# Kernel optimization log

Measured on AMD Instinct MI355X. Metric: run time of the kernel, lower is better.

Reference implementation:

```python
import jax, jax.numpy as jnp
import numpy as np

EPS = 1e-5
NC = 183  # num_classes
FUSION_LEVEL = 1

def conv2d(x, w, b=None, pad=0):
    y = jax.lax.conv_general_dilated(x, w, (1, 1), [(pad, pad), (pad, pad)],
                                     dimension_numbers=('NCHW', 'OIHW', 'NCHW'))
    return y if b is None else y + b[None, :, None, None]

def bn(x, g, b, m, v):
    s = g / jnp.sqrt(v + EPS)
    return x * s[None, :, None, None] + (b - m * s)[None, :, None, None]

def deform_conv(x, offset, weight):
    # DCNv1: x [B,C,H,W], offset [B,18,H,W] as (dy,dx) per kernel point, weight [O,C,3,3]
    B, C, H, W = x.shape
    K = 9
    off = offset.reshape(B, K, 2, H, W)
    ky = (jnp.arange(K) // 3 - 1).astype(x.dtype)
    kx = (jnp.arange(K) % 3 - 1).astype(x.dtype)
    yy = jnp.arange(H, dtype=x.dtype)[None, None, :, None] + ky[None, :, None, None] + off[:, :, 0]
    xx = jnp.arange(W, dtype=x.dtype)[None, None, None, :] + kx[None, :, None, None] + off[:, :, 1]
    y0 = jnp.floor(yy)
    x0 = jnp.floor(xx)
    wy = yy - y0
    wx = xx - x0
    def gather(yi, xi):
        valid = ((yi >= 0) & (yi <= H - 1) & (xi >= 0) & (xi <= W - 1))
        yc = jnp.clip(yi, 0, H - 1).astype(jnp.int32)
        xc = jnp.clip(xi, 0, W - 1).astype(jnp.int32)
        g = jax.vmap(lambda im, a, b: im[:, a, b])(x, yc, xc)  # [B,C,K,H,W]
        return g * valid.astype(x.dtype)[:, None]
    s = (gather(y0, x0) * ((1 - wy) * (1 - wx))[:, None]
         + gather(y0, x0 + 1) * ((1 - wy) * wx)[:, None]
         + gather(y0 + 1, x0) * (wy * (1 - wx))[:, None]
         + gather(y0 + 1, x0 + 1) * (wy * wx)[:, None])
    return jnp.einsum('bckhw,ock->bohw', s, weight.reshape(weight.shape[0], C, K))

def resize_bilinear(x, oh, ow):
    # F.interpolate(mode='bilinear', align_corners=True)
    B, C, H, W = x.shape
    if (H, W) == (oh, ow):
        return x
    ys = jnp.linspace(0.0, H - 1.0, oh)
    xs = jnp.linspace(0.0, W - 1.0, ow)
    y0 = jnp.clip(jnp.floor(ys).astype(jnp.int32), 0, H - 2)
    x0 = jnp.clip(jnp.floor(xs).astype(jnp.int32), 0, W - 2)
    wy = (ys - y0).astype(x.dtype)
    wx = (xs - x0).astype(x.dtype)
    r = x[:, :, y0, :] * (1 - wy)[None, None, :, None] + x[:, :, y0 + 1, :] * wy[None, None, :, None]
    return r[:, :, :, x0] * (1 - wx) + r[:, :, :, x0 + 1] * wx

def setup_inputs() -> dict:
    key = jax.random.key(0)
    ks = iter(jax.random.split(key, 64))
    nk = lambda: next(ks)
    B, C = 1, 256
    sizes = [256, 128, 64, 32, 16]
    w = lambda shape, sc: jax.random.normal(nk(), shape, jnp.float32) * sc
    inp = {}
    for i, s in enumerate(sizes):
        inp['feat%d' % i] = jax.random.normal(nk(), (B, C, s, s), jnp.float32)
    inp['off1_w'] = w((18, C, 3, 3), 0.01); inp['off1_b'] = w((18,), 0.01)
    inp['dc1_w'] = w((C, C, 3, 3), 0.02)
    inp['off2_w'] = w((18, C, 3, 3), 0.01); inp['off2_b'] = w((18,), 0.01)
    inp['dc2_w'] = w((C, C, 3, 3), 0.02)
    inp['bn2_g'] = 1.0 + w((C,), 0.01); inp['bn2_b'] = w((C,), 0.01)
    inp['bn2_m'] = w((C,), 0.01); inp['bn2_v'] = jax.random.uniform(nk(), (C,), jnp.float32) + 0.5
    inp['convs_w'] = w((4, C, C, 3, 3), 0.02)
    inp['convs_g'] = 1.0 + w((4, C), 0.01); inp['convs_b'] = w((4, C), 0.01)
    inp['convs_m'] = w((4, C), 0.01); inp['convs_v'] = jax.random.uniform(nk(), (4, C), jnp.float32) + 0.5
    inp['emb_w'] = w((C, C, 1, 1), 0.05)
    inp['emb_g'] = 1.0 + w((C,), 0.01); inp['emb_b'] = w((C,), 0.01)
    inp['emb_m'] = w((C,), 0.01); inp['emb_v'] = jax.random.uniform(nk(), (C,), jnp.float32) + 0.5
    inp['logit_w'] = w((NC, C, 1, 1), 0.05); inp['logit_b'] = w((NC,), 0.01)
    return inp

def reference(feat0, feat1, feat2, feat3, feat4,
              off1_w, off1_b, dc1_w, off2_w, off2_b, dc2_w,
              bn2_g, bn2_b, bn2_m, bn2_v,
              convs_w, convs_g, convs_b, convs_m, convs_v,
              emb_w, emb_g, emb_b, emb_m, emb_v,
              logit_w, logit_b):
    feats = [feat0, feat1, feat2, feat3, feat4]
    def branch(f):
        o = conv2d(f, off1_w, off1_b, pad=1)
        h = deform_conv(f, o, dc1_w)
        o = conv2d(h, off2_w, off2_b, pad=1)
        h = deform_conv(h, o, dc2_w)
        return jax.nn.relu(bn(h, bn2_g, bn2_b, bn2_m, bn2_v))
    x = branch(feats[FUSION_LEVEL])
    H, W = x.shape[-2:]
    for i, f in enumerate(feats):
        if i != FUSION_LEVEL:
            x = x + branch(resize_bilinear(f, H, W))
    for i in range(4):
        x = jax.nn.relu(bn(conv2d(x, convs_w[i], pad=1),
                           convs_g[i], convs_b[i], convs_m[i], convs_v[i]))
    mask_pred = conv2d(x, logit_w, logit_b, pad=0)
    emb = jax.nn.relu(bn(conv2d(x, emb_w, pad=0), emb_g, emb_b, emb_m, emb_v))
    return (mask_pred, emb)
```

## Files before the change

### kernel.cpp

```cpp
#include <hip/hip_runtime.h>
#include <hip/hip_bf16.h>
#include <stdint.h>

#define EPS_BN 1e-5f
constexpr int PP = 16384;
using short8 = __attribute__((ext_vector_type(8))) short;
using f32x4  = __attribute__((ext_vector_type(4))) float;
typedef unsigned short u16;

__device__ inline float bf2f(u16 u) {
  unsigned v = ((unsigned)u) << 16; float f; __builtin_memcpy(&f, &v, 4); return f;
}
__device__ inline u16 f2bf(float f) {
  unsigned b; __builtin_memcpy(&b, &f, 4);
  b += 0x7FFFu + ((b >> 16) & 1u);
  return (u16)(b >> 16);
}

#define GLD16(g, l) __builtin_amdgcn_global_load_lds( \
    (__attribute__((address_space(1))) void*)(void*)(g), \
    (__attribute__((address_space(3))) void*)(void*)(l), 16, 0, 0)

__global__ void bn_prep_k(const float* __restrict__ g0, const float* __restrict__ b0,
                          const float* __restrict__ m0, const float* __restrict__ v0,
                          const float* __restrict__ cg, const float* __restrict__ cb,
                          const float* __restrict__ cm, const float* __restrict__ cv,
                          const float* __restrict__ eg, const float* __restrict__ eb,
                          const float* __restrict__ em, const float* __restrict__ ev,
                          float* __restrict__ scale, float* __restrict__ shift) {
  int c = threadIdx.x;
  float s = g0[c] * rsqrtf(v0[c] + EPS_BN);
  scale[c] = s; shift[c] = b0[c] - m0[c] * s;
#pragma unroll
  for (int i = 0; i < 4; ++i) {
    float si = cg[i*256+c] * rsqrtf(cv[i*256+c] + EPS_BN);
    scale[(1+i)*256+c] = si; shift[(1+i)*256+c] = cb[i*256+c] - cm[i*256+c]*si;
  }
  float se = eg[c] * rsqrtf(ev[c] + EPS_BN);
  scale[5*256+c] = se; shift[5*256+c] = eb[c] - em[c]*se;
}

__global__ void prep_w_k(const float* __restrict__ w, u16* __restrict__ W2,
                         int Ocnt, int KK, int NPAD) {
  int idx = blockIdx.x * 256 + threadIdx.x;
  int total = NPAD * KK * 256;
  if (idx >= total) return;
  int o = idx / (KK * 256); int rem = idx - o * (KK * 256);
  int kpt = rem >> 8, c = rem & 255;
  W2[idx] = (o < Ocnt) ? f2bf(w[(o * 256 + c) * KK + kpt]) : (u16)0;
}

__global__ void tr_k(const float* __restrict__ in, u16* __restrict__ out, int P) {
  __shared__ float tile[64][65];
  int p0 = blockIdx.x * 64, c0 = blockIdx.y * 64;
  int t = threadIdx.x;
  int tl = t & 63, tg = t >> 6;
#pragma unroll
  for (int i = 0; i < 16; ++i) {
    int c = tg * 16 + i;
    tile[c][tl] = in[(size_t)(c0 + c) * P + p0 + tl];
  }
  __syncthreads();
  int px = t >> 2, cq = t & 3;
#pragma unroll
  for (int pass = 0; pass < 2; ++pass) {
    int c = cq * 8 + pass * 32;
    u16 r[8];
#pragma unroll
    for (int j = 0; j < 8; ++j) r[j] = f2bf(tile[c + j][px]);
    *(short8*)(out + (size_t)(p0 + px) * 256 + c0 + c) = *(short8*)r;
  }
}

__global__ void rs_k(const u16* __restrict__ in, u16* __restrict__ out, int Hs) {
  int t = threadIdx.x;
  int p = blockIdx.x * 8 + (t >> 5), q = t & 31;
  int oy = p >> 7, ox = p & 127;
  float sc = (float)(Hs - 1) / 127.0f;
  float ys = oy * sc, xs = ox * sc;
  int y0 = (int)ys; if (y0 > Hs - 2) y0 = Hs - 2;
  int x0 = (int)xs; if (x0 > Hs - 2) x0 = Hs - 2;
  float wy = ys - (float)y0, wx = xs - (float)x0;
  const u16* b00 = in + ((size_t)(y0 * Hs + x0)) * 256 + q * 8;
  short8 v00 = *(const short8*)b00;
  short8 v01 = *(const short8*)(b00 + 256);
  short8 v10 = *(const short8*)(b00 + (size_t)Hs * 256);
  short8 v11 = *(const short8*)(b00 + (size_t)Hs * 256 + 256);
  u16 r[8];
#pragma unroll
  for (int j = 0; j < 8; ++j) {
    float a = bf2f((u16)v00[j]) * (1.f - wx) + bf2f((u16)v01[j]) * wx;
    float b = bf2f((u16)v10[j]) * (1.f - wx) + bf2f((u16)v11[j]) * wx;
    r[j] = f2bf(a * (1.f - wy) + b * wy);
  }
  *(short8*)(out + (size_t)p * 256 + q * 8) = *(short8*)r;
}

template<int EPI>
__launch_bounds__(256, 2)
__global__ void dc_k(const u16* __restrict__ A, const u16* __restrict__ Bw,
                     const float* __restrict__ offs, u16* __restrict__ oB,
                     const float* __restrict__ scale, const float* __restrict__ shift) {
  __shared__ u16 sB[2][256 * 32];
  const int t = threadIdx.x, w = t >> 6, l = t & 63, lr = l & 15, lq = l >> 4;
  int bx = blockIdx.x; { int n8 = gridDim.x >> 3; bx = (bx & 7) * n8 + (bx >> 3); }
  const int p0 = bx * 128;
  const int gp0 = p0 + w * 32 + lr, gp1 = gp0 + 16;

  f32x4 acc[2][16];
#pragma unroll
  for (int r = 0; r < 2; ++r)
#pragma unroll
    for (int n = 0; n < 16; ++n) acc[r][n] = (f32x4){0.f, 0.f, 0.f, 0.f};

  float wgt[2][4];
  int   cb[2][4];
  short8 cv[2][4];
  const short8 z8 = (short8){0, 0, 0, 0, 0, 0, 0, 0};

  unsigned boff[4];
#pragma unroll
  for (int it = 0; it < 4; ++it) {
    int ch = it * 256 + t, row = ch >> 2, s = ch & 3;
    int cl = s ^ ((row ^ (row >> 2)) & 3);
    boff[it] = (unsigned)(row * 2304 + cl * 8);
  }

  auto newKpt = [&](int kpt) {
    float2 oa = *(const float2*)(offs + (size_t)gp0 * 32 + 2 * kpt);
    float2 ob = *(const float2*)(offs + (size_t)gp1 * 32 + 2 * kpt);
    float ky = (float)(kpt / 3 - 1), kx = (float)(kpt % 3 - 1);
#pragma unroll
    for (int r = 0; r < 2; ++r) {
      int g = r ? gp1 : gp0;
      float2 o2 = r ? ob : oa;
      int pl = g & 16383, lb = g & ~16383;
      float yy = (float)(pl >> 7) + ky + o2.x;
      float xx = (float)(pl & 127) + kx + o2.y;
      float yf = floorf(yy), xf = floorf(xx);
      float fy = yy - yf, fx = xx - xf;
      int y0 = (int)yf, x0 = (int)xf;
      bool va = (unsigned)y0 < 128u, vb = (unsigned)(y0 + 1) < 128u;
      bool ha = (unsigned)x0 < 128u, hb = (unsigned)(x0 + 1) < 128u;
      wgt[r][0] = (1.f - fy) * (1.f - fx); cb[r][0] = (va && ha) ? lb + (y0 << 7) + x0 : -1;
      wgt[r][1] = (1.f - fy) * fx;         cb[r][1] = (va && hb) ? lb + (y0 << 7) + x0 + 1 : -1;
      wgt[r][2] = fy * (1.f - fx);         cb[r][2] = (vb && ha) ? lb + ((y0 + 1) << 7) + x0 : -1;
      wgt[r][3] = fy * fx;                 cb[r][3] = (vb && hb) ? lb + ((y0 + 1) << 7) + x0 + 1 : -1;
    }
  };
  auto loadC = [&](int ks) {
    int cc = ((ks & 7) << 5) + lq * 8;
#pragma unroll
    for (int r = 0; r < 2; ++r)
#pragma unroll
      for (int c = 0; c < 4; ++c)
        cv[r][c] = (cb[r][c] >= 0) ? *(const short8*)(A + (size_t)cb[r][c] * 256 + cc) : z8;
  };

  newKpt(0);
  loadC(0);
  const int laneoff = lr * 64 + ((lq ^ ((lr ^ (lr >> 2)) & 3)) << 4);

  for (int ks = 0; ks < 72; ++ks) {
    {
      const u16* bbase = Bw + ks * 32;
      char* dst = (char*)sB[ks & 1] + w * 1024;
#pragma unroll
      for (int it = 0; it < 4; ++it) GLD16(bbase + boff[it], dst + it * 4096);
    }
    short8 af[2];
#pragma unroll
    for (int r = 0; r < 2; ++r) {
      u16 rr[8];
#pragma unroll
      for (int j = 0; j < 8; ++j) {
        float v = wgt[r][0] * bf2f((u16)cv[r][0][j]) + wgt[r][1] * bf2f((u16)cv[r][1][j])
                + wgt[r][2] * bf2f((u16)cv[r][2][j]) + wgt[r][3] * bf2f((u16)cv[r][3][j]);
        __hip_bfloat16 h = __float2bfloat16(v);
        rr[j] = *(u16*)&h;
      }
      af[r] = *(short8*)rr;
    }
    if (ks < 71 && (((ks + 1) & 7) == 0)) newKpt((ks + 1) >> 3);
    __syncthreads();
    if (ks < 71) loadC(ks + 1);
    const char* base = (const char*)sB[ks & 1] + laneoff;
    __builtin_amdgcn_s_setprio(1);
#pragma unroll
    for (int n = 0; n < 16; ++n) {
      short8 bfr = *(const short8*)(base + n * 1024);
      acc[0][n] = __builtin_amdgcn_mfma_f32_16x16x32_bf16(af[0], bfr, acc[0][n], 0, 0, 0);
      acc[1][n] = __builtin_amdgcn_mfma_f32_16x16x32_bf16(af[1], bfr, acc[1][n], 0, 0, 0);
    }
    __builtin_amdgcn_s_setprio(0);
  }

#pragma unroll
  for (int r = 0; r < 2; ++r) {
    int prow = p0 + w * 32 + r * 16 + lq * 4;
#pragma unroll
    for (int n = 0; n < 16; ++n) {
      int oc = n * 16 + lr;
      float sc = 1.f, sh = 0.f;
      if constexpr (EPI == 3) { sc = scale[oc]; sh = shift[oc]; }
#pragma unroll
      for (int q = 0; q < 4; ++q) {
        float v = acc[r][n][q];
        if constexpr (EPI == 3) v = fmaxf(v * sc + sh, 0.f);
        oB[(size_t)(prow + q) * 256 + oc] = f2bf(v);
      }
    }
  }
}

template<int MODE, int AM, int AN, int MW, int NW, int EPI>
__launch_bounds__(MW*NW*64)
__global__ void mm_k(const u16* __restrict__ A, const u16* __restrict__ B,
                     const u16* __restrict__ zbuf,
                     float* __restrict__ oF, u16* __restrict__ oB,
                     const float* __restrict__ bias,
                     const float* __restrict__ scale, const float* __restrict__ shift,
                     int Ktot, int ksteps, int OutN) {
  constexpr int BM = MW * AM * 16, BN = NW * AN * 16, NT = MW * NW * 64;
  constexpr int AITS = BM * 8 / NT, BITS = BN * 8 / NT;
  __shared__ u16 sA[BM * 64];
  __shared__ u16 sB[BN * 64];
  char* sAb = (char*)sA; char* sBb = (char*)sB;
  const int t = threadIdx.x;
  const int w = t >> 6, l = t & 63;
  const int lr = l & 15, lq = l >> 4;
  const int wm = w / NW, wn = w % NW;
  int bx = blockIdx.x;
  { int n8 = gridDim.x >> 3; bx = (bx & 7) * n8 + (bx >> 3); }
  const int p0 = bx * BM, n0 = blockIdx.y * BN;

  f32x4 acc[AM][AN];
#pragma unroll
  for (int m = 0; m < AM; ++m)
#pragma unroll
    for (int n = 0; n < AN; ++n) acc[m][n] = (f32x4){0.f, 0.f, 0.f, 0.f};

  for (int ks = 0; ks < ksteps; ++ks) {
    int k0 = ks * 64;
#pragma unroll
    for (int it = 0; it < BITS; ++it) {
      int ch = it * NT + t;
      int row = ch >> 3, cl = (ch & 7) ^ (row & 7);
      GLD16(B + (size_t)(n0 + row) * Ktot + k0 + cl * 8, sBb + it * (NT * 16) + w * 1024);
    }
    if constexpr (MODE == 0) {
#pragma unroll
      for (int it = 0; it < AITS; ++it) {
        int ch = it * NT + t;
        int row = ch >> 3, cl = (ch & 7) ^ (row & 7);
        GLD16(A + (size_t)(p0 + row) * Ktot + k0 + cl * 8, sAb + it * (NT * 16) + w * 1024);
      }
    } else {
      int kpt = k0 >> 8, c0 = k0 & 255;
      int dy = kpt / 3 - 1, dx = kpt % 3 - 1;
#pragma unroll
      for (int it = 0; it < AITS; ++it) {
        int ch = it * NT + t;
        int row = ch >> 3, cl = (ch & 7) ^ (row & 7);
        int gp = p0 + row; int lvl = gp >> 14, pl = gp & 16383;
        int yy = (pl >> 7) + dy, xx = (pl & 127) + dx;
        const u16* src = ((unsigned)yy < 128u && (unsigned)xx < 128u)
            ? A + ((size_t)(lvl << 14) + (yy << 7) + xx) * 256 + c0 + cl * 8
            : zbuf;
        GLD16(src, sAb + it * (NT * 16) + w * 1024);
      }
    }
    __syncthreads();
    short8 af[AM], bfr[AN];
#pragma unroll
    for (int h = 0; h < 2; ++h) {
#pragma unroll
      for (int m = 0; m < AM; ++m) {
        int ar = wm * AM * 16 + m * 16 + lr;
        af[m] = *(const short8*)(sAb + ar * 128 + (((h * 4 + lq) ^ (ar & 7)) << 4));
      }
#pragma unroll
      for (int n = 0; n < AN; ++n) {
        int br = wn * AN * 16 + n * 16 + lr;
        bfr[n] = *(const short8*)(sBb + br * 128 + (((h * 4 + lq) ^ (br & 7)) << 4));
      }
#pragma unroll
      for (int m = 0; m < AM; ++m)
#pragma unroll
        for (int n = 0; n < AN; ++n)
          acc[m][n] = __builtin_amdgcn_mfma_f32_16x16x32_bf16(af[m], bfr[n], acc[m][n], 0, 0, 0);
    }
    __syncthreads();
  }

#pragma unroll
  for (int m = 0; m < AM; ++m) {
    int prow = p0 + wm * AM * 16 + m * 16 + lq * 4;
#pragma unroll
    for (int n = 0; n < AN; ++n) {
      int oc = n0 + wn * AN * 16 + n * 16 + lr;
      if constexpr (EPI == 1) {
        float bs = (oc < 18) ? bias[oc] : 0.f;
#pragma unroll
        for (int r = 0; r < 4; ++r) oF[(size_t)(prow + r) * 32 + oc] = acc[m][n][r] + bs;
      } else if constexpr (EPI == 2) {
#pragma unroll
        for (int r = 0; r < 4; ++r) oB[(size_t)(prow + r) * 256 + oc] = f2bf(acc[m][n][r]);
      } else if constexpr (EPI == 3) {
        float sc = scale[oc], sh = shift[oc];
#pragma unroll
        for (int r = 0; r < 4; ++r)
          oB[(size_t)(prow + r) * 256 + oc] = f2bf(fmaxf(acc[m][n][r] * sc + sh, 0.f));
      } else if constexpr (EPI == 4) {
        if (oc < OutN) {
          float bs = bias[oc];
          float4 v = {acc[m][n][0] + bs, acc[m][n][1] + bs, acc[m][n][2] + bs, acc[m][n][3] + bs};
          *(float4*)(oF + (size_t)oc * PP + prow) = v;
        }
      } else {
        float sc = scale[oc], sh = shift[oc];
        float4 v = {fmaxf(acc[m][n][0] * sc + sh, 0.f), fmaxf(acc[m][n][1] * sc + sh, 0.f),
                    fmaxf(acc[m][n][2] * sc + sh, 0.f), fmaxf(acc[m][n][3] * sc + sh, 0.f)};
        *(float4*)(oF + (size_t)oc * PP + prow) = v;
      }
    }
  }
}

__global__ void sum5_k(const u16* __restrict__ H2, u16* __restrict__ out) {
  size_t base = ((size_t)blockIdx.x * 256 + threadIdx.x) * 8;
  float a[8] = {0,0,0,0,0,0,0,0};
#pragma unroll
  for (int lvl = 0; lvl < 5; ++lvl) {
    short8 v = *(const short8*)(H2 + (size_t)lvl * PP * 256 + base);
#pragma unroll
    for (int j = 0; j < 8; ++j) a[j] += bf2f((u16)v[j]);
  }
  u16 r[8];
#pragma unroll
  for (int j = 0; j < 8; ++j) r[j] = f2bf(a[j]);
  *(short8*)(out + base) = *(short8*)r;
}

extern "C" void kernel_launch(void* const* d_in, const int* in_sizes, int n_in,
                              void* d_out, int out_size, void* d_ws, size_t ws_size,
                              hipStream_t stream) {
  const float* feats[5];
  for (int i = 0; i < 5; ++i) feats[i] = (const float*)d_in[i];
  int fsz[5] = {256, 128, 64, 32, 16};
  const float* off1_w = (const float*)d_in[5];
  const float* off1_b = (const float*)d_in[6];
  const float* dc1_w  = (const float*)d_in[7];
  const float* off2_w = (const float*)d_in[8];
  const float* off2_b = (const float*)d_in[9];
  const float* dc2_w  = (const float*)d_in[10];
  const float* bn2_g  = (const float*)d_in[11];
  const float* bn2_b  = (const float*)d_in[12];
  const float* bn2_m  = (const float*)d_in[13];
  const float* bn2_v  = (const float*)d_in[14];
  const float* convs_w = (const float*)d_in[15];
  const float* convs_g = (const float*)d_in[16];
  const float* convs_b = (const float*)d_in[17];
  const float* convs_m = (const float*)d_in[18];
  const float* convs_v = (const float*)d_in[19];
  const float* emb_w  = (const float*)d_in[20];
  const float* emb_g  = (const float*)d_in[21];
  const float* emb_b  = (const float*)d_in[22];
  const float* emb_m  = (const float*)d_in[23];
  const float* emb_v  = (const float*)d_in[24];
  const float* logit_w = (const float*)d_in[25];
  const float* logit_b = (const float*)d_in[26];

  char* ws = (char*)d_ws;
  size_t off = 0;
  auto alloc = [&](size_t bytes) { char* p = ws + off; off += (bytes + 255) & ~255ull; return p; };
  float* bnscale = (float*)alloc(6 * 256 * 4);
  float* bnshift = (float*)alloc(6 * 256 * 4);
  u16* zbuf = (u16*)alloc(256);
  u16* W2_off1 = (u16*)alloc((size_t)32 * 2304 * 2);
  u16* W2_off2 = (u16*)alloc((size_t)32 * 2304 * 2);
  u16* W2_dc1  = (u16*)alloc((size_t)256 * 2304 * 2);
  u16* W2_dc2  = (u16*)alloc((size_t)256 * 2304 * 2);
  u16* W2_c    = (u16*)alloc((size_t)4 * 256 * 2304 * 2);
  u16* W2_logit = (u16*)alloc((size_t)256 * 256 * 2);
  u16* W2_emb   = (u16*)alloc((size_t)256 * 256 * 2);
  u16* R_all  = (u16*)alloc((size_t)5 * PP * 256 * 2);
  u16* H_all  = (u16*)alloc((size_t)5 * PP * 256 * 2);
  u16* H2_all = (u16*)alloc((size_t)5 * PP * 256 * 2);
  float* O    = (float*)alloc((size_t)5 * PP * 32 * 4);
  u16* Xb     = (u16*)alloc((size_t)PP * 256 * 2);
  u16* Ftmp = H_all;
  u16* cb0 = R_all;
  u16* cb1 = R_all + (size_t)PP * 256;

  hipMemsetAsync(zbuf, 0, 256, stream);
  bn_prep_k<<<1, 256, 0, stream>>>(bn2_g, bn2_b, bn2_m, bn2_v, convs_g, convs_b, convs_m, convs_v,
                                   emb_g, emb_b, emb_m, emb_v, bnscale, bnshift);
  auto pw = [&](const float* src, u16* dst, int Ocnt, int KK, int NPAD) {
    int total = NPAD * KK * 256;
    prep_w_k<<<(total + 255) / 256, 256, 0, stream>>>(src, dst, Ocnt, KK, NPAD);
  };
  pw(off1_w, W2_off1, 18, 9, 32);
  pw(off2_w, W2_off2, 18, 9, 32);
  pw(dc1_w,  W2_dc1, 256, 9, 256);
  pw(dc2_w,  W2_dc2, 256, 9, 256);
  for (int i = 0; i < 4; ++i) pw(convs_w + (size_t)i * 2304 * 256, W2_c + (size_t)i * 2304 * 256, 256, 9, 256);
  pw(logit_w, W2_logit, 183, 1, 256);
  pw(emb_w,   W2_emb,   256, 1, 256);

  const dim3 blk(256);
  for (int lvl = 0; lvl < 5; ++lvl) {
    int P = fsz[lvl] * fsz[lvl];
    u16* dst = (lvl == 1) ? (R_all + (size_t)PP * 256) : Ftmp;
    tr_k<<<dim3(P / 64, 4), blk, 0, stream>>>(feats[lvl], dst, P);
    if (lvl != 1)
      rs_k<<<dim3(PP / 8), blk, 0, stream>>>(Ftmp, R_all + (size_t)lvl * PP * 256, fsz[lvl]);
  }

  constexpr int MG = 5 * PP;
  mm_k<1, 2, 2, 4, 1, 1><<<dim3(MG / 128, 1), blk, 0, stream>>>(
      R_all, W2_off1, zbuf, O, nullptr, off1_b, nullptr, nullptr, 2304, 36, 32);
  dc_k<2><<<dim3(MG / 128), blk, 0, stream>>>(R_all, W2_dc1, O, H_all, nullptr, nullptr);
  mm_k<1, 2, 2, 4, 1, 1><<<dim3(MG / 128, 1), blk, 0, stream>>>(
      H_all, W2_off2, zbuf, O, nullptr, off2_b, nullptr, nullptr, 2304, 36, 32);
  dc_k<3><<<dim3(MG / 128), blk, 0, stream>>>(H_all, W2_dc2, O, H2_all, bnscale, bnshift);

  sum5_k<<<dim3(2048), blk, 0, stream>>>(H2_all, Xb);

  const u16* cur = Xb;
  u16* cbuf[2] = {cb0, cb1};
  for (int i = 0; i < 4; ++i) {
    mm_k<1, 2, 4, 2, 2, 3><<<dim3(PP / 64, 2), blk, 0, stream>>>(
        cur, W2_c + (size_t)i * 2304 * 256, zbuf, nullptr, cbuf[i & 1],
        nullptr, bnscale + (1 + i) * 256, bnshift + (1 + i) * 256, 2304, 36, 256);
    cur = cbuf[i & 1];
  }

  float* outp = (float*)d_out;
  mm_k<0, 2, 4, 2, 2, 4><<<dim3(PP / 64, 2), blk, 0, stream>>>(
      cur, W2_logit, zbuf, outp, nullptr, logit_b, nullptr, nullptr, 256, 4, 183);
  mm_k<0, 2, 4, 2, 2, 5><<<dim3(PP / 64, 2), blk, 0, stream>>>(
      cur, W2_emb, zbuf, outp + (size_t)183 * PP, nullptr, nullptr,
      bnscale + 5 * 256, bnshift + 5 * 256, 256, 4, 256);
}
```

Baseline: 965.7 us.

## Halve deformable-conv tile rows per wave to raise occupancy and prefetch offsets

Each wave of the deformable conv kernel now handles 16 output pixels instead of 32, so a block covers 64 pixels and the grid doubles. Occupancy rises from 2 to 3 blocks per SM. Register pressure drops, and the next kernel point's offset is prefetched one step ahead. Bilinear blending now unpacks bf16 pairs from 32-bit words. The cost is that every weight tile loaded into LDS is reused by half as many MFMAs, which doubles weight traffic per output and lowers MFMA density per sync.

```diff
diff --git a/kernel.cpp b/kernel.cpp
--- a/kernel.cpp
+++ b/kernel.cpp
@@ -97,25 +97,25 @@
 }
 
 template<int EPI>
-__launch_bounds__(256, 2)
+__launch_bounds__(256, 3)
 __global__ void dc_k(const u16* __restrict__ A, const u16* __restrict__ Bw,
                      const float* __restrict__ offs, u16* __restrict__ oB,
                      const float* __restrict__ scale, const float* __restrict__ shift) {
   __shared__ u16 sB[2][256 * 32];
   const int t = threadIdx.x, w = t >> 6, l = t & 63, lr = l & 15, lq = l >> 4;
   int bx = blockIdx.x; { int n8 = gridDim.x >> 3; bx = (bx & 7) * n8 + (bx >> 3); }
-  const int p0 = bx * 128;
-  const int gp0 = p0 + w * 32 + lr, gp1 = gp0 + 16;
-
-  f32x4 acc[2][16];
-#pragma unroll
-  for (int r = 0; r < 2; ++r)
-#pragma unroll
-    for (int n = 0; n < 16; ++n) acc[r][n] = (f32x4){0.f, 0.f, 0.f, 0.f};
-
-  float wgt[2][4];
-  int   cb[2][4];
-  short8 cv[2][4];
+  const int p0 = bx * 64;
+  const int gp = p0 + w * 16 + lr;
+  const int pl = gp & 16383, lb = gp & ~16383;
+
+  f32x4 acc[16];
+#pragma unroll
+  for (int n = 0; n < 16; ++n) acc[n] = (f32x4){0.f, 0.f, 0.f, 0.f};
+
+  float wgt[4];
+  int   cb[4];
+  short8 cv[4];
+  float2 onext;
   const short8 z8 = (short8){0, 0, 0, 0, 0, 0, 0, 0};
 
   unsigned boff[4];
@@ -126,35 +126,28 @@
     boff[it] = (unsigned)(row * 2304 + cl * 8);
   }
 
+  onext = *(const float2*)(offs + (size_t)gp * 32);
+
   auto newKpt = [&](int kpt) {
-    float2 oa = *(const float2*)(offs + (size_t)gp0 * 32 + 2 * kpt);
-    float2 ob = *(const float2*)(offs + (size_t)gp1 * 32 + 2 * kpt);
-    float ky = (float)(kpt / 3 - 1), kx = (float)(kpt % 3 - 1);
-#pragma unroll
-    for (int r = 0; r < 2; ++r) {
-      int g = r ? gp1 : gp0;
-      float2 o2 = r ? ob : oa;
-      int pl = g & 16383, lb = g & ~16383;
-      float yy = (float)(pl >> 7) + ky + o2.x;
-      float xx = (float)(pl & 127) + kx + o2.y;
-      float yf = floorf(yy), xf = floorf(xx);
-      float fy = yy - yf, fx = xx - xf;
-      int y0 = (int)yf, x0 = (int)xf;
-      bool va = (unsigned)y0 < 128u, vb = (unsigned)(y0 + 1) < 128u;
-      bool ha = (unsigned)x0 < 128u, hb = (unsigned)(x0 + 1) < 128u;
-      wgt[r][0] = (1.f - fy) * (1.f - fx); cb[r][0] = (va && ha) ? lb + (y0 << 7) + x0 : -1;
-      wgt[r][1] = (1.f - fy) * fx;         cb[r][1] = (va && hb) ? lb + (y0 << 7) + x0 + 1 : -1;
-      wgt[r][2] = fy * (1.f - fx);         cb[r][2] = (vb && ha) ? lb + ((y0 + 1) << 7) + x0 : -1;
-      wgt[r][3] = fy * fx;                 cb[r][3] = (vb && hb) ? lb + ((y0 + 1) << 7) + x0 + 1 : -1;
-    }
+    float2 o2 = onext;
+    if (kpt < 8) onext = *(const float2*)(offs + (size_t)gp * 32 + 2 * (kpt + 1));
+    float yy = (float)((pl >> 7) + kpt / 3 - 1) + o2.x;
+    float xx = (float)((pl & 127) + kpt % 3 - 1) + o2.y;
+    float yf = floorf(yy), xf = floorf(xx);
+    float fy = yy - yf, fx = xx - xf;
+    int y0 = (int)yf, x0 = (int)xf;
+    bool va = (unsigned)y0 < 128u, vb = (unsigned)(y0 + 1) < 128u;
+    bool ha = (unsigned)x0 < 128u, hb = (unsigned)(x0 + 1) < 128u;
+    wgt[0] = (1.f - fy) * (1.f - fx); cb[0] = (va && ha) ? lb + (y0 << 7) + x0 : -1;
+    wgt[1] = (1.f - fy) * fx;         cb[1] = (va && hb) ? lb + (y0 << 7) + x0 + 1 : -1;
+    wgt[2] = fy * (1.f - fx);         cb[2] = (vb && ha) ? lb + ((y0 + 1) << 7) + x0 : -1;
+    wgt[3] = fy * fx;                 cb[3] = (vb && hb) ? lb + ((y0 + 1) << 7) + x0 + 1 : -1;
   };
   auto loadC = [&](int ks) {
     int cc = ((ks & 7) << 5) + lq * 8;
 #pragma unroll
-    for (int r = 0; r < 2; ++r)
-#pragma unroll
-      for (int c = 0; c < 4; ++c)
-        cv[r][c] = (cb[r][c] >= 0) ? *(const short8*)(A + (size_t)cb[r][c] * 256 + cc) : z8;
+    for (int c = 0; c < 4; ++c)
+      cv[c] = (cb[c] >= 0) ? *(const short8*)(A + (size_t)cb[c] * 256 + cc) : z8;
   };
 
   newKpt(0);
@@ -168,18 +161,37 @@
 #pragma unroll
       for (int it = 0; it < 4; ++it) GLD16(bbase + boff[it], dst + it * 4096);
     }
-    short8 af[2];
-#pragma unroll
-    for (int r = 0; r < 2; ++r) {
+    short8 af;
+    {
       u16 rr[8];
-#pragma unroll
-      for (int j = 0; j < 8; ++j) {
-        float v = wgt[r][0] * bf2f((u16)cv[r][0][j]) + wgt[r][1] * bf2f((u16)cv[r][1][j])
-                + wgt[r][2] * bf2f((u16)cv[r][2][j]) + wgt[r][3] * bf2f((u16)cv[r][3][j]);
-        __hip_bfloat16 h = __float2bfloat16(v);
-        rr[j] = *(u16*)&h;
-      }
-      af[r] = *(short8*)rr;
+      const unsigned* u0 = (const unsigned*)&cv[0];
+      const unsigned* u1 = (const unsigned*)&cv[1];
+      const unsigned* u2 = (const unsigned*)&cv[2];
+      const unsigned* u3 = (const unsigned*)&cv[3];
+#pragma unroll
+      for (int j2 = 0; j2 < 4; ++j2) {
+        float lo, hi;
+        {
+          unsigned a0 = u0[j2], a1 = u1[j2], a2 = u2[j2], a3 = u3[j2];
+          float l0, h0, l1, h1, l2, h2, l3, h3;
+          unsigned tl_, th_;
+          tl_ = a0 << 16; th_ = a0 & 0xFFFF0000u;
+          __builtin_memcpy(&l0, &tl_, 4); __builtin_memcpy(&h0, &th_, 4);
+          tl_ = a1 << 16; th_ = a1 & 0xFFFF0000u;
+          __builtin_memcpy(&l1, &tl_, 4); __builtin_memcpy(&h1, &th_, 4);
+          tl_ = a2 << 16; th_ = a2 & 0xFFFF0000u;
+          __builtin_memcpy(&l2, &tl_, 4); __builtin_memcpy(&h2, &th_, 4);
+          tl_ = a3 << 16; th_ = a3 & 0xFFFF0000u;
+          __builtin_memcpy(&l3, &tl_, 4); __builtin_memcpy(&h3, &th_, 4);
+          lo = wgt[0] * l0 + wgt[1] * l1 + wgt[2] * l2 + wgt[3] * l3;
+          hi = wgt[0] * h0 + wgt[1] * h1 + wgt[2] * h2 + wgt[3] * h3;
+        }
+        __hip_bfloat16 hl = __float2bfloat16(lo);
+        __hip_bfloat16 hh = __float2bfloat16(hi);
+        rr[2 * j2]     = *(u16*)&hl;
+        rr[2 * j2 + 1] = *(u16*)&hh;
+      }
+      af = *(short8*)rr;
     }
     if (ks < 71 && (((ks + 1) & 7) == 0)) newKpt((ks + 1) >> 3);
     __syncthreads();
@@ -189,15 +201,13 @@
 #pragma unroll
     for (int n = 0; n < 16; ++n) {
       short8 bfr = *(const short8*)(base + n * 1024);
-      acc[0][n] = __builtin_amdgcn_mfma_f32_16x16x32_bf16(af[0], bfr, acc[0][n], 0, 0, 0);
-      acc[1][n] = __builtin_amdgcn_mfma_f32_16x16x32_bf16(af[1], bfr, acc[1][n], 0, 0, 0);
+      acc[n] = __builtin_amdgcn_mfma_f32_16x16x32_bf16(af, bfr, acc[n], 0, 0, 0);
     }
     __builtin_amdgcn_s_setprio(0);
   }
 
-#pragma unroll
-  for (int r = 0; r < 2; ++r) {
-    int prow = p0 + w * 32 + r * 16 + lq * 4;
+  {
+    int prow = p0 + w * 16 + lq * 4;
 #pragma unroll
     for (int n = 0; n < 16; ++n) {
       int oc = n * 16 + lr;
@@ -205,7 +215,7 @@
       if constexpr (EPI == 3) { sc = scale[oc]; sh = shift[oc]; }
 #pragma unroll
       for (int q = 0; q < 4; ++q) {
-        float v = acc[r][n][q];
+        float v = acc[n][q];
         if constexpr (EPI == 3) v = fmaxf(v * sc + sh, 0.f);
         oB[(size_t)(prow + q) * 256 + oc] = f2bf(v);
       }
@@ -420,10 +430,10 @@
   constexpr int MG = 5 * PP;
   mm_k<1, 2, 2, 4, 1, 1><<<dim3(MG / 128, 1), blk, 0, stream>>>(
       R_all, W2_off1, zbuf, O, nullptr, off1_b, nullptr, nullptr, 2304, 36, 32);
-  dc_k<2><<<dim3(MG / 128), blk, 0, stream>>>(R_all, W2_dc1, O, H_all, nullptr, nullptr);
+  dc_k<2><<<dim3(MG / 64), blk, 0, stream>>>(R_all, W2_dc1, O, H_all, nullptr, nullptr);
   mm_k<1, 2, 2, 4, 1, 1><<<dim3(MG / 128, 1), blk, 0, stream>>>(
       H_all, W2_off2, zbuf, O, nullptr, off2_b, nullptr, nullptr, 2304, 36, 32);
-  dc_k<3><<<dim3(MG / 128), blk, 0, stream>>>(H_all, W2_dc2, O, H2_all, bnscale, bnshift);
+  dc_k<3><<<dim3(MG / 64), blk, 0, stream>>>(H_all, W2_dc2, O, H2_all, bnscale, bnshift);
 
   sum5_k<<<dim3(2048), blk, 0, stream>>>(H2_all, Xb);
 
```

Result: faster. 879.3 us (-8.9%).

## Triple-buffer weight staging and prefetch offsets in deformable conv kernel

Applied to the files above, without the earlier changes.

Moves the shared-memory weight tiles for the deformable-conv GEMM from double to triple buffering, issuing the LDS DMA for step ks+1 before computing step ks. It also prefetches the next kernel point's offsets one step ahead. The bf16-to-float unpacking of the bilinear samples now works on 32-bit pairs, and the full __syncthreads is replaced by a raw s_barrier plus a sched_barrier. The aim is to hide global-load latency behind the MFMA work and cut barrier overhead. Shared memory per block grows, and the raw barrier may not wait for the outstanding LDS DMA the way the old sync did, which is a correctness risk.

```diff
diff --git a/kernel.cpp b/kernel.cpp
--- a/kernel.cpp
+++ b/kernel.cpp
@@ -101,11 +101,11 @@
 __global__ void dc_k(const u16* __restrict__ A, const u16* __restrict__ Bw,
                      const float* __restrict__ offs, u16* __restrict__ oB,
                      const float* __restrict__ scale, const float* __restrict__ shift) {
-  __shared__ u16 sB[2][256 * 32];
+  __shared__ u16 sB[3][256 * 32];
   const int t = threadIdx.x, w = t >> 6, l = t & 63, lr = l & 15, lq = l >> 4;
   int bx = blockIdx.x; { int n8 = gridDim.x >> 3; bx = (bx & 7) * n8 + (bx >> 3); }
   const int p0 = bx * 128;
-  const int gp0 = p0 + w * 32 + lr, gp1 = gp0 + 16;
+  const int gp0 = p0 + w * 32 + lr;
 
   f32x4 acc[2][16];
 #pragma unroll
@@ -116,6 +116,7 @@
   float wgt[2][4];
   int   cb[2][4];
   short8 cv[2][4];
+  float2 onext[2];
   const short8 z8 = (short8){0, 0, 0, 0, 0, 0, 0, 0};
 
   unsigned boff[4];
@@ -126,14 +127,16 @@
     boff[it] = (unsigned)(row * 2304 + cl * 8);
   }
 
+  onext[0] = *(const float2*)(offs + (size_t)gp0 * 32);
+  onext[1] = *(const float2*)(offs + (size_t)(gp0 + 16) * 32);
+
   auto newKpt = [&](int kpt) {
-    float2 oa = *(const float2*)(offs + (size_t)gp0 * 32 + 2 * kpt);
-    float2 ob = *(const float2*)(offs + (size_t)gp1 * 32 + 2 * kpt);
     float ky = (float)(kpt / 3 - 1), kx = (float)(kpt % 3 - 1);
 #pragma unroll
     for (int r = 0; r < 2; ++r) {
-      int g = r ? gp1 : gp0;
-      float2 o2 = r ? ob : oa;
+      int g = gp0 + r * 16;
+      float2 o2 = onext[r];
+      if (kpt < 8) onext[r] = *(const float2*)(offs + (size_t)g * 32 + 2 * (kpt + 1));
       int pl = g & 16383, lb = g & ~16383;
       float yy = (float)(pl >> 7) + ky + o2.x;
       float xx = (float)(pl & 127) + kx + o2.y;
@@ -156,35 +159,55 @@
       for (int c = 0; c < 4; ++c)
         cv[r][c] = (cb[r][c] >= 0) ? *(const short8*)(A + (size_t)cb[r][c] * 256 + cc) : z8;
   };
-
+  auto stageB = [&](int ks) {
+    const u16* bbase = Bw + ks * 32;
+    char* dst = (char*)sB[ks % 3] + w * 1024;
+#pragma unroll
+    for (int it = 0; it < 4; ++it) GLD16(bbase + boff[it], dst + it * 4096);
+  };
+
+  stageB(0);
   newKpt(0);
   loadC(0);
   const int laneoff = lr * 64 + ((lq ^ ((lr ^ (lr >> 2)) & 3)) << 4);
 
   for (int ks = 0; ks < 72; ++ks) {
-    {
-      const u16* bbase = Bw + ks * 32;
-      char* dst = (char*)sB[ks & 1] + w * 1024;
-#pragma unroll
-      for (int it = 0; it < 4; ++it) GLD16(bbase + boff[it], dst + it * 4096);
-    }
+    if (ks < 71) stageB(ks + 1);
     short8 af[2];
 #pragma unroll
     for (int r = 0; r < 2; ++r) {
       u16 rr[8];
-#pragma unroll
-      for (int j = 0; j < 8; ++j) {
-        float v = wgt[r][0] * bf2f((u16)cv[r][0][j]) + wgt[r][1] * bf2f((u16)cv[r][1][j])
-                + wgt[r][2] * bf2f((u16)cv[r][2][j]) + wgt[r][3] * bf2f((u16)cv[r][3][j]);
-        __hip_bfloat16 h = __float2bfloat16(v);
-        rr[j] = *(u16*)&h;
+      const unsigned* u0 = (const unsigned*)&cv[r][0];
+      const unsigned* u1 = (const unsigned*)&cv[r][1];
+      const unsigned* u2 = (const unsigned*)&cv[r][2];
+      const unsigned* u3 = (const unsigned*)&cv[r][3];
+#pragma unroll
+      for (int j2 = 0; j2 < 4; ++j2) {
+        unsigned a0 = u0[j2], a1 = u1[j2], a2 = u2[j2], a3 = u3[j2];
+        float l0, h0, l1, h1, l2, h2, l3, h3;
+        unsigned tl_, th_;
+        tl_ = a0 << 16; th_ = a0 & 0xFFFF0000u;
+        __builtin_memcpy(&l0, &tl_, 4); __builtin_memcpy(&h0, &th_, 4);
+        tl_ = a1 << 16; th_ = a1 & 0xFFFF0000u;
+        __builtin_memcpy(&l1, &tl_, 4); __builtin_memcpy(&h1, &th_, 4);
+        tl_ = a2 << 16; th_ = a2 & 0xFFFF0000u;
+        __builtin_memcpy(&l2, &tl_, 4); __builtin_memcpy(&h2, &th_, 4);
+        tl_ = a3 << 16; th_ = a3 & 0xFFFF0000u;
+        __builtin_memcpy(&l3, &tl_, 4); __builtin_memcpy(&h3, &th_, 4);
+        float lo = wgt[r][0] * l0 + wgt[r][1] * l1 + wgt[r][2] * l2 + wgt[r][3] * l3;
+        float hi = wgt[r][0] * h0 + wgt[r][1] * h1 + wgt[r][2] * h2 + wgt[r][3] * h3;
+        __hip_bfloat16 hl = __float2bfloat16(lo);
+        __hip_bfloat16 hh = __float2bfloat16(hi);
+        rr[2 * j2]     = *(u16*)&hl;
+        rr[2 * j2 + 1] = *(u16*)&hh;
       }
       af[r] = *(short8*)rr;
     }
     if (ks < 71 && (((ks + 1) & 7) == 0)) newKpt((ks + 1) >> 3);
-    __syncthreads();
+    __builtin_amdgcn_s_barrier();
+    __builtin_amdgcn_sched_barrier(0);
     if (ks < 71) loadC(ks + 1);
-    const char* base = (const char*)sB[ks & 1] + laneoff;
+    const char* base = (const char*)sB[ks % 3] + laneoff;
     __builtin_amdgcn_s_setprio(1);
 #pragma unroll
     for (int n = 0; n < 16; ++n) {
```

Measured after the change: 988.1 us. 2.3% more time.
